# Kernel tuning notes

Hardware: AMD Instinct MI355X
Metric: run time of the kernel (lower is better)

## Reference

```python
import jax, jax.numpy as jnp
import numpy as np

N = 50000
E = 800000
NFEAT = 128
NHID = 32
HEADS = 8
NCLASS = 40


def _gat_conv(x, src, dst, W, att_src, att_dst, bias, concat):
    # x: [N, Fin]; W: [Fin, H*C]; att_*: [H, C]; bias: [H*C] or [C]
    n = x.shape[0]
    H, C = att_src.shape
    h = (x @ W).reshape(n, H, C)                      # [N,H,C]
    a_src = (h * att_src[None]).sum(-1)               # [N,H]
    a_dst = (h * att_dst[None]).sum(-1)               # [N,H]
    e = jax.nn.leaky_relu(a_src[src] + a_dst[dst], 0.2)  # [E,H]
    # edge softmax over incoming edges of each dst node
    m = jax.ops.segment_max(e, dst, num_segments=n)   # [N,H]
    e = jnp.exp(e - m[dst])
    s = jax.ops.segment_sum(e, dst, num_segments=n)   # [N,H]
    alpha = e / (s[dst] + 1e-16)                      # [E,H]
    msg = h[src] * alpha[:, :, None]                  # [E,H,C]
    out = jax.ops.segment_sum(msg, dst, num_segments=n)  # [N,H,C]
    if concat:
        out = out.reshape(n, H * C)
    else:
        out = out.mean(axis=1)
    return out + bias


def setup_inputs() -> dict:
    key = jax.random.key(0)
    ks = jax.random.split(key, 10)
    x = jax.random.normal(ks[0], (N, NFEAT), dtype=jnp.float32)
    edge_index = jax.random.randint(ks[1], (2, E), 0, N, dtype=jnp.int64)
    sc = 1.0 / np.sqrt(NFEAT)
    W1 = jax.random.uniform(ks[2], (NFEAT, HEADS * NHID), jnp.float32, -sc, sc)
    a1_src = jax.random.uniform(ks[3], (HEADS, NHID), jnp.float32, -sc, sc)
    a1_dst = jax.random.uniform(ks[4], (HEADS, NHID), jnp.float32, -sc, sc)
    b1 = jnp.zeros((HEADS * NHID,), jnp.float32)
    sc2 = 1.0 / np.sqrt(HEADS * NHID)
    W2 = jax.random.uniform(ks[5], (HEADS * NHID, NCLASS), jnp.float32, -sc2, sc2)
    a2_src = jax.random.uniform(ks[6], (1, NCLASS), jnp.float32, -sc2, sc2)
    a2_dst = jax.random.uniform(ks[7], (1, NCLASS), jnp.float32, -sc2, sc2)
    b2 = jnp.zeros((NCLASS,), jnp.float32)
    return {"x": x, "edge_index": edge_index, "W1": W1, "a1_src": a1_src,
            "a1_dst": a1_dst, "b1": b1, "W2": W2, "a2_src": a2_src,
            "a2_dst": a2_dst, "b2": b2}


def reference(x, edge_index, W1, a1_src, a1_dst, b1, W2, a2_src, a2_dst, b2):
    n = x.shape[0]
    loop = jnp.arange(n, dtype=edge_index.dtype)
    src = jnp.concatenate([edge_index[0], loop])  # add self-loops (PyG default)
    dst = jnp.concatenate([edge_index[1], loop])
    # dropout layers are identity in eval mode
    h = jax.nn.elu(_gat_conv(x, src, dst, W1, a1_src, a1_dst, b1, concat=True))
    out = _gat_conv(h, src, dst, W2, a2_src, a2_dst, b2, concat=False)
    return jax.nn.log_softmax(out, axis=1)
```

## Files before the change

### kernel.cpp

```cpp
#include <hip/hip_runtime.h>
#include <math.h>

#define NFEAT  128
#define HC     256
#define HEADS  8
#define NHID   32
#define NCLASS 40

#define INV_LN2 1.44269504088896340736f

typedef unsigned int  uint;
typedef unsigned short ushort;
typedef unsigned char uchar;

typedef __attribute__((ext_vector_type(8))) short bf16x8;
typedef __attribute__((ext_vector_type(4))) float f32x4;
typedef __attribute__((ext_vector_type(2))) float f32x2;

union U8 { uint4 u; bf16x8 v; };

__device__ __forceinline__ uint f2bf1(float f) {
    uint b = __float_as_uint(f);
    b += 0x7FFFu + ((b >> 16) & 1u);
    return b >> 16;
}
__device__ __forceinline__ uint packbf(float lo, float hi) {
    return f2bf1(lo) | (f2bf1(hi) << 16);
}

__device__ __forceinline__ uchar f2fp8(float v) {
    return (uchar)(__builtin_amdgcn_cvt_pk_fp8_f32(v, v, 0, false) & 0xFF);
}
__device__ __forceinline__ float fp8tof(uint byte) {
    auto v2 = __builtin_amdgcn_cvt_pk_f32_fp8((int)byte, false);
    return v2[0];
}

__device__ __forceinline__ float bperm(int addr, float v) {
    return __int_as_float(__builtin_amdgcn_ds_bpermute(addr, __float_as_int(v)));
}
__device__ __forceinline__ int bperm_i(int addr, int v) {
    return __builtin_amdgcn_ds_bpermute(addr, v);
}

#define HU 8
#define PREPB 23
__global__ __launch_bounds__(256)
void k_hist_prep(const int* __restrict__ dst, int E, int* deg,
                 int* __restrict__ rank,
                 const float* __restrict__ W1,
                 const float* __restrict__ attS, const float* __restrict__ attD,
                 const float* __restrict__ W2,
                 const float* __restrict__ a2sw, const float* __restrict__ a2dw,
                 ushort* __restrict__ Wb1, ushort* __restrict__ Wb2) {
    int blk = blockIdx.x;
    int t = threadIdx.x;
    if (blk >= PREPB) {
        int tid = (blk - PREPB) * 256 + t;
        int stride = (gridDim.x - PREPB) * 256;
#pragma unroll
        for (int j = 0; j < HU; ++j) {
            int i = tid + j * stride;
            if (i < E) rank[i] = atomicAdd(&deg[dst[i]], 1);
        }
        return;
    }
    float f[8];
    if (blk < 17) {
        int g = blk * 256 + t;
        int lane = g & 63;
        int step = (g >> 6) & 3;
        int tile = g >> 8;
        int k0 = step * 32 + (lane >> 4) * 8;
        if (tile < 16) {
            int ncol = tile * 16 + (lane & 15);
#pragma unroll
            for (int j = 0; j < 8; ++j) f[j] = W1[(size_t)(k0 + j) * HC + ncol];
        } else {
            int cc = lane & 15;
            int h = cc & 7;
            const float* av = (cc < 8) ? attS : attD;
#pragma unroll
            for (int j = 0; j < 8; ++j) {
                const float* wr = W1 + (size_t)(k0 + j) * HC + h * 32;
                float s = 0.f;
#pragma unroll
                for (int c = 0; c < 32; ++c) s += wr[c] * av[h * 32 + c];
                f[j] = s * INV_LN2;
            }
        }
        uint4 o;
        o.x = packbf(f[0], f[1]);
        o.y = packbf(f[2], f[3]);
        o.z = packbf(f[4], f[5]);
        o.w = packbf(f[6], f[7]);
        *(uint4*)(Wb1 + (size_t)g * 8) = o;
    } else {
        int g = (blk - 17) * 256 + t;
        if (g >= 3 * 8 * 64) return;
        int lane = g & 63;
        int ks = (g >> 6) & 7;
        int nt = g >> 9;
        int cc = lane & 15;
        int ncol = nt * 16 + cc;
        int k0 = ks * 32 + (lane >> 4) * 8;
        if (ncol < NCLASS) {
#pragma unroll
            for (int j = 0; j < 8; ++j) f[j] = W2[(size_t)(k0 + j) * NCLASS + ncol];
        } else if (ncol <= 41) {
            const float* av = (ncol == 40) ? a2sw : a2dw;
#pragma unroll
            for (int j = 0; j < 8; ++j) {
                const float* wr = W2 + (size_t)(k0 + j) * NCLASS;
                float s = 0.f;
#pragma unroll
                for (int c = 0; c < NCLASS; ++c) s += wr[c] * av[c];
                f[j] = s * INV_LN2;
            }
        } else {
#pragma unroll
            for (int j = 0; j < 8; ++j) f[j] = 0.f;
        }
        uint4 o;
        o.x = packbf(f[0], f[1]);
        o.y = packbf(f[2], f[3]);
        o.z = packbf(f[4], f[5]);
        o.w = packbf(f[6], f[7]);
        *(uint4*)(Wb2 + (size_t)g * 8) = o;
    }
}

#define SU 4
__global__ __launch_bounds__(256)
void k_scatter_gemm1(const int* __restrict__ srcE, const int* __restrict__ dstE,
                     const int* __restrict__ rank, int E,
                     int* __restrict__ srcs, int scb,
                     const float* __restrict__ x, const ushort* __restrict__ Wb,
                     int n, uchar* __restrict__ h1f8, float* __restrict__ a1x) {
    __shared__ uint Xs[64 * 68];
    int t = threadIdx.x;
    if (blockIdx.x < scb) {
        int tid = blockIdx.x * 256 + t;
        int stride = scb * 256;
        int P = (E + 3) >> 2;
#pragma unroll
        for (int g = 0; g < SU; ++g) {
            int pk = tid + g * stride;
            if (pk >= P) continue;
            int i0 = pk * 4;
            if (i0 + 4 <= E) {
                int4 d4 = *(const int4*)(dstE + i0);
                int4 r4 = *(const int4*)(rank + i0);
                int4 s4 = *(const int4*)(srcE + i0);
                if (r4.x < 64) srcs[((size_t)d4.x << 6) + r4.x] = s4.x;
                if (r4.y < 64) srcs[((size_t)d4.y << 6) + r4.y] = s4.y;
                if (r4.z < 64) srcs[((size_t)d4.z << 6) + r4.z] = s4.z;
                if (r4.w < 64) srcs[((size_t)d4.w << 6) + r4.w] = s4.w;
            } else {
                for (int i = i0; i < E; ++i) {
                    int r = rank[i];
                    if (r < 64) srcs[((size_t)dstE[i] << 6) + r] = srcE[i];
                }
            }
        }
        return;
    }
    int lane = t & 63;
    int w = t >> 6;
    int n0 = (blockIdx.x - scb) * 64;

#pragma unroll
    for (int j = 0; j < 8; ++j) {
        int f4 = t + j * 256;
        int node = f4 >> 5;
        int k4 = (f4 & 31) * 4;
        int gn = n0 + node;
        float4 v = make_float4(0.f, 0.f, 0.f, 0.f);
        if (gn < n) v = *(const float4*)(x + (size_t)gn * NFEAT + k4);
        uint2 pk;
        pk.x = packbf(v.x, v.y);
        pk.y = packbf(v.z, v.w);
        *(uint2*)(Xs + node * 68 + (k4 >> 1)) = pk;
    }
    __syncthreads();

    int m = lane & 15;
    int q4 = (lane >> 4) * 4;
    bf16x8 Af[4];
#pragma unroll
    for (int ks = 0; ks < 4; ++ks) {
        U8 a;
        a.u = *(const uint4*)(Xs + (w * 16 + m) * 68 + ks * 16 + q4);
        Af[ks] = a.v;
    }
    __syncthreads();

    f32x4 acc[17];
#pragma unroll
    for (int i = 0; i < 17; ++i) acc[i] = (f32x4){0.f, 0.f, 0.f, 0.f};

    const bf16x8* Bf = (const bf16x8*)Wb;
#pragma unroll
    for (int ks = 0; ks < 4; ++ks) {
#pragma unroll
        for (int nt = 0; nt < 17; ++nt) {
            bf16x8 bv = Bf[(size_t)(nt * 4 + ks) * 64 + lane];
            acc[nt] = __builtin_amdgcn_mfma_f32_16x16x32_bf16(Af[ks], bv, acc[nt], 0, 0, 0);
        }
    }

    int cc = lane & 15;
    int r0 = (lane >> 4) * 4;

#pragma unroll
    for (int r = 0; r < 4; ++r) {
        int gn = n0 + w * 16 + r0 + r;
        if (gn < n) a1x[(size_t)gn * 16 + cc] = acc[16][r];
    }

    uchar* CsB = (uchar*)Xs;
#pragma unroll
    for (int nt = 0; nt < 16; ++nt) {
#pragma unroll
        for (int r = 0; r < 4; ++r)
            CsB[(w * 16 + r0 + r) * 272 + nt * 16 + cc] = f2fp8(acc[nt][r]);
    }
    __syncthreads();

    int node_local = t >> 2;
    int q = t & 3;
    int gn = n0 + node_local;
    if (gn < n) {
        const uchar* crow = CsB + node_local * 272 + q * 64;
        uchar* hp = h1f8 + (size_t)gn * HC + q * 64;
#pragma unroll
        for (int i = 0; i < 4; ++i)
            *(uint4*)(hp + i * 16) = *(const uint4*)(crow + i * 16);
    }
}

__global__ __launch_bounds__(256)
void k_agg1(const uint* __restrict__ h1u, const float* __restrict__ a1x,
            const float* __restrict__ b1, const int* __restrict__ deg,
            const int* __restrict__ srcs,
            int n, ushort* __restrict__ hgb) {
    int wid = blockIdx.x * 4 + (threadIdx.x >> 6);
    if (wid >= n) return;
    wid = __builtin_amdgcn_readfirstlane(wid);
    int lane = threadIdx.x & 63;
    int vj = lane >> 3;
    int hh = lane & 7;
    int hacc = lane >> 3;
    float adn = a1x[(size_t)wid * 16 + 8 + hh];
    const char* a1xb = (const char*)a1x;
    int ax8  = (lane ^ 8)  << 2;
    int ax16 = (lane ^ 16) << 2;
    int ax32 = (lane ^ 32) << 2;
    int bpc  = hacc << 2;
    int bpp[8];
#pragma unroll
    for (int j = 0; j < 8; ++j) bpp[j] = ((j << 3) + hacc) << 2;

    int degw = __builtin_amdgcn_readfirstlane(deg[wid]);
    degw = (degw < 63) ? degw : 63;
    int cnt = degw + 1;
    int sv_full = srcs[((size_t)wid << 6) + lane];
    int sv_pad = (lane < degw) ? sv_full : wid;

    float s = 0.f;
    f32x2 acc01 = (f32x2){0.f, 0.f};
    f32x2 acc23 = (f32x2){0.f, 0.f};

    struct Chunk { float av; uint hv[8]; };
    Chunk A, B;

#define LOADC1(C, base) do {                                                   \
    int idxl_ = (base) + vj;                                                   \
    int svv_ = bperm_i(idxl_ << 2, sv_pad);                                    \
    (C).av = *(const float*)(a1xb + ((size_t)(uint)svv_ << 6) + ((uint)hh << 2)); \
    _Pragma("unroll")                                                          \
    for (int j_ = 0; j_ < 8; ++j_) {                                           \
        if ((base) + j_ >= cnt) break;                     \
        int sn_ = __builtin_amdgcn_readlane(sv_pad, (base) + j_);              \
        (C).hv[j_] = h1u[(size_t)(uint)sn_ * 64 + lane];                       \
    }                                                                          \
} while (0)

#define CONSC1(C, base) do {                                                   \
    int idxl_ = (base) + vj;                                                   \
    float a_ = (C).av + adn;                                                   \
    float e_ = fmaxf(a_, 0.2f * a_);                                           \
    float p_ = (idxl_ < cnt) ? __builtin_exp2f(e_) : 0.f;                      \
    s += p_;                                                                   \
    _Pragma("unroll")                                                          \
    for (int j_ = 0; j_ < 8; ++j_) {                                           \
        if ((base) + j_ >= cnt) break;                     \
        float pj_ = bperm(bpp[j_], p_);                                        \
        f32x2 pj2_ = (f32x2){pj_, pj_};                                        \
        auto lo_ = __builtin_amdgcn_cvt_pk_f32_fp8((int)(C).hv[j_], false);    \
        auto hi_ = __builtin_amdgcn_cvt_pk_f32_fp8((int)(C).hv[j_], true);     \
        f32x2 lov_ = (f32x2){lo_[0], lo_[1]};                                  \
        f32x2 hiv_ = (f32x2){hi_[0], hi_[1]};                                  \
        acc01 += pj2_ * lov_;                                                  \
        acc23 += pj2_ * hiv_;                                                  \
    }                                                                          \
} while (0)

    int i = 0;
    LOADC1(A, 0);
    while (i + 8 < cnt) {
        LOADC1(B, i + 8);
        CONSC1(A, i);
        i += 8;
        if (i + 8 < cnt) {
            LOADC1(A, i + 8);
            CONSC1(B, i);
            i += 8;
        } else {
            CONSC1(B, i);
            goto tail1;
        }
    }
    CONSC1(A, i);
tail1:;
#undef LOADC1
#undef CONSC1

    float ps = s + bperm(ax8, s);
    ps += bperm(ax16, ps);
    ps += bperm(ax32, ps);
    float inv = 1.f / (ps + 1e-16f);
    float inv_a = bperm(bpc, inv);
    float4 bv = *(const float4*)(b1 + lane * 4);
    float4 o;
    o.x = acc01[0] * inv_a + bv.x;
    o.y = acc01[1] * inv_a + bv.y;
    o.z = acc23[0] * inv_a + bv.z;
    o.w = acc23[1] * inv_a + bv.w;
    o.x = (o.x > 0.f) ? o.x : (__expf(o.x) - 1.f);
    o.y = (o.y > 0.f) ? o.y : (__expf(o.y) - 1.f);
    o.z = (o.z > 0.f) ? o.z : (__expf(o.z) - 1.f);
    o.w = (o.w > 0.f) ? o.w : (__expf(o.w) - 1.f);
    uint2 ov;
    ov.x = packbf(o.x, o.y);
    ov.y = packbf(o.z, o.w);
    *(uint2*)(hgb + (size_t)wid * HC + lane * 4) = ov;
}

__global__ __launch_bounds__(256)
void k_gemm2(const ushort* __restrict__ hgb, const ushort* __restrict__ Wb2,
             int n, uchar* __restrict__ h2f8) {
    __shared__ uint Xs[64 * 132];
    int t = threadIdx.x;
    int lane = t & 63;
    int w = t >> 6;
    int n0 = blockIdx.x * 64;

#pragma unroll
    for (int j = 0; j < 8; ++j) {
        int g = t + j * 256;
        int node = g >> 5;
        int u4 = g & 31;
        int gn = n0 + node;
        uint4 v = make_uint4(0u, 0u, 0u, 0u);
        if (gn < n) v = *(const uint4*)(hgb + (size_t)gn * HC + u4 * 8);
        *(uint4*)(Xs + node * 132 + u4 * 4) = v;
    }
    __syncthreads();

    int m = lane & 15;
    int q4 = (lane >> 4) * 4;
    bf16x8 Af[8];
#pragma unroll
    for (int ks = 0; ks < 8; ++ks) {
        U8 a;
        a.u = *(const uint4*)(Xs + (w * 16 + m) * 132 + ks * 16 + q4);
        Af[ks] = a.v;
    }
    __syncthreads();

    f32x4 acc[3];
#pragma unroll
    for (int i = 0; i < 3; ++i) acc[i] = (f32x4){0.f, 0.f, 0.f, 0.f};

    const bf16x8* Bf = (const bf16x8*)Wb2;
#pragma unroll
    for (int ks = 0; ks < 8; ++ks) {
#pragma unroll
        for (int nt = 0; nt < 3; ++nt) {
            bf16x8 bv = Bf[(size_t)(nt * 8 + ks) * 64 + lane];
            acc[nt] = __builtin_amdgcn_mfma_f32_16x16x32_bf16(Af[ks], bv, acc[nt], 0, 0, 0);
        }
    }

    int cc = lane & 15;
    int r0 = (lane >> 4) * 4;

    uchar* CsB = (uchar*)Xs;
#pragma unroll
    for (int nt = 0; nt < 2; ++nt) {
#pragma unroll
        for (int r = 0; r < 4; ++r)
            CsB[(w * 16 + r0 + r) * 64 + nt * 16 + cc] = f2fp8(acc[nt][r]);
    }
#pragma unroll
    for (int r = 0; r < 4; ++r) {
        int row = (w * 16 + r0 + r) * 64;
        if (cc < 8)       CsB[row + 32 + cc] = f2fp8(acc[2][r]);
        else if (cc == 8) *(float*)(CsB + row + 40) = acc[2][r];
        else if (cc == 9) *(float*)(CsB + row + 44) = acc[2][r];
        else if (cc == 10) *(uint*)(CsB + row + 48) = 0u;
        else if (cc == 11) *(uint*)(CsB + row + 52) = 0u;
        else if (cc == 12) *(uint*)(CsB + row + 56) = 0u;
        else if (cc == 13) *(uint*)(CsB + row + 60) = 0u;
    }
    __syncthreads();

    int node_local = t >> 2;
    int q = t & 3;
    int gn = n0 + node_local;
    if (gn < n)
        *(uint4*)(h2f8 + (size_t)gn * 64 + q * 16) =
            *(const uint4*)(CsB + node_local * 64 + q * 16);
}

__global__ __launch_bounds__(256)
void k_agg2(const uchar* __restrict__ h2f8, const float* __restrict__ b2,
            const int* __restrict__ deg, const int* __restrict__ srcs,
            int n, float* __restrict__ out) {
    int wid = blockIdx.x * 4 + (threadIdx.x >> 6);
    if (wid >= n) return;
    wid = __builtin_amdgcn_readfirstlane(wid);
    int lane = threadIdx.x & 63;
    int vj = lane & 7;
    bool live = lane < NCLASS;
    int col = live ? lane : 0;
    const char* h2b = (const char*)h2f8;
    float adn = *(const float*)(h2b + (size_t)wid * 64 + 44);
    int ax1 = (lane ^ 1) << 2;
    int ax2 = (lane ^ 2) << 2;
    int ax4 = (lane ^ 4) << 2;
    int bpj[8];
#pragma unroll
    for (int j = 0; j < 8; ++j) bpj[j] = j << 2;

    int degw = __builtin_amdgcn_readfirstlane(deg[wid]);
    degw = (degw < 63) ? degw : 63;
    int cnt = degw + 1;
    int sv_full = srcs[((size_t)wid << 6) + lane];
    int sv_pad = (lane < degw) ? sv_full : wid;

    float s = 0.f, acc = 0.f;

    struct Chunk2 { float av; uint hb[8]; };
    Chunk2 A, B;

#define LOADC2(C, base) do {                                                   \
    int idxl_ = (base) + vj;                                                   \
    int svv_ = bperm_i(idxl_ << 2, sv_pad);                                    \
    (C).av = *(const float*)(h2b + ((size_t)(uint)svv_ << 6) + 40u);           \
    _Pragma("unroll")                                                          \
    for (int j_ = 0; j_ < 8; ++j_) {                                           \
        if ((base) + j_ >= cnt) break;                     \
        int sn_ = __builtin_amdgcn_readlane(sv_pad, (base) + j_);              \
        (C).hb[j_] = h2f8[(size_t)(uint)sn_ * 64 + col];                       \
    }                                                                          \
} while (0)

#define CONSC2(C, base) do {                                                   \
    int idxl_ = (base) + vj;                                                   \
    float a_ = (C).av + adn;                                                   \
    float e_ = fmaxf(a_, 0.2f * a_);                                           \
    float p_ = (idxl_ < cnt) ? __builtin_exp2f(e_) : 0.f;                      \
    s += p_;                                                                   \
    _Pragma("unroll")                                                          \
    for (int j_ = 0; j_ < 8; ++j_) {                                           \
        if ((base) + j_ >= cnt) break;                     \
        float pj_ = bperm(bpj[j_], p_);                                        \
        acc += pj_ * fp8tof((C).hb[j_]);                                       \
    }                                                                          \
} while (0)

    int i = 0;
    LOADC2(A, 0);
    while (i + 8 < cnt) {
        LOADC2(B, i + 8);
        CONSC2(A, i);
        i += 8;
        if (i + 8 < cnt) {
            LOADC2(A, i + 8);
            CONSC2(B, i);
            i += 8;
        } else {
            CONSC2(B, i);
            goto tail2;
        }
    }
    CONSC2(A, i);
tail2:;
#undef LOADC2
#undef CONSC2

    float ps = s + bperm(ax1, s);
    ps += bperm(ax2, ps);
    ps += bperm(ax4, ps);

    float val0 = acc / (ps + 1e-16f) + (live ? b2[lane] : 0.f);
    float vmax = live ? val0 : -INFINITY;
#pragma unroll
    for (int msk = 1; msk < 64; msk <<= 1) vmax = fmaxf(vmax, __shfl_xor(vmax, msk, 64));
    float ex = live ? __expf(val0 - vmax) : 0.f;
#pragma unroll
    for (int msk = 1; msk < 64; msk <<= 1) ex += __shfl_xor(ex, msk, 64);
    float res = val0 - vmax - __logf(ex);
    if (live) out[(size_t)wid * NCLASS + lane] = res;
}

extern "C" void kernel_launch(void* const* d_in, const int* in_sizes, int n_in,
                              void* d_out, int out_size, void* d_ws, size_t ws_size,
                              hipStream_t stream) {
    const float* x    = (const float*)d_in[0];
    const int*   ei   = (const int*)  d_in[1];
    const float* W1   = (const float*)d_in[2];
    const float* attS = (const float*)d_in[3];
    const float* attD = (const float*)d_in[4];
    const float* b1   = (const float*)d_in[5];
    const float* W2   = (const float*)d_in[6];
    const float* a2sw = (const float*)d_in[7];
    const float* a2dw = (const float*)d_in[8];
    const float* b2   = (const float*)d_in[9];

    int n = in_sizes[0] / NFEAT;
    int E = in_sizes[1] / 2;
    const int* srcE = ei;
    const int* dstE = ei + E;
    int mblocks = (n + 63) / 64;

    char* p = (char*)d_ws;
    auto alloc = [&](size_t bytes) {
        char* r = p;
        p += (bytes + 255) & ~(size_t)255;
        return r;
    };
    uchar*  h1f8 = (uchar*)alloc((size_t)n * HC);
    ushort* hgb  = (ushort*)alloc((size_t)n * HC * 2);
    uchar*  h2f8 = (uchar*)alloc((size_t)n * 64);
    ushort* Wb1  = (ushort*)alloc((size_t)17 * 4 * 64 * 8 * 2);
    ushort* Wb2  = (ushort*)alloc((size_t)3 * 8 * 64 * 8 * 2);
    float* a1x = (float*)alloc((size_t)n * 16 * 4);
    int* deg  = (int*)alloc((size_t)n * 4);
    int* rank = (int*)alloc((size_t)E * 4);
    int* srcs = (int*)alloc((size_t)n * 64 * 4);

    int histb = (E + 256 * HU - 1) / (256 * HU);
    int P = (E + 3) / 4;
    int scb = (P + 256 * SU - 1) / (256 * SU);
    hipMemsetAsync(deg, 0, (size_t)n * 4, stream);
    k_hist_prep<<<PREPB + histb, 256, 0, stream>>>(dstE, E, deg, rank,
                                                   W1, attS, attD, W2, a2sw, a2dw,
                                                   Wb1, Wb2);
    k_scatter_gemm1<<<scb + mblocks, 256, 0, stream>>>(
        srcE, dstE, rank, E, srcs, scb, x, Wb1, n, h1f8, a1x);
    k_agg1<<<(n + 3) / 4, 256, 0, stream>>>((const uint*)h1f8, a1x, b1,
                                            deg, srcs, n, hgb);
    k_gemm2<<<mblocks, 256, 0, stream>>>(hgb, Wb2, n, h2f8);
    k_agg2<<<(n + 3) / 4, 256, 0, stream>>>(h2f8, b2, deg, srcs, n, (float*)d_out);
}
```

Before: 226.5 us.

## Fuse histogram and scatter into a partitioned single pass; triple-buffer aggregation loads

Replaces the two-pass edge bucketing (an atomic histogram that writes ranks, then a separate scatter pass) with one pass. Each block group owns one eighth of the destination-node range, so atomics and srcs writes stay local, and the rank array is removed. The scatter is split out of the GEMM1 launch into its own gemm1 kernel. Both aggregation kernels move from double to triple buffering of neighbor chunks with prefetch two ahead, and the per-element count-break checks are dropped because padded lanes carry self indices. The cost is that every group re-reads the whole edge list, eight reads in total, and the extra chunk buffer adds register pressure.

```diff
diff --git a/kernel.cpp b/kernel.cpp
--- a/kernel.cpp
+++ b/kernel.cpp
@@ -43,11 +43,12 @@
     return __builtin_amdgcn_ds_bpermute(addr, v);
 }
 
-#define HU 8
+
 #define PREPB 23
+#define SCG 125
 __global__ __launch_bounds__(256)
-void k_hist_prep(const int* __restrict__ dst, int E, int* deg,
-                 int* __restrict__ rank,
+void k_hist_prep(const int* __restrict__ srcE, const int* __restrict__ dstE,
+                 int E, int n, int* deg, int* __restrict__ srcs,
                  const float* __restrict__ W1,
                  const float* __restrict__ attS, const float* __restrict__ attD,
                  const float* __restrict__ W2,
@@ -56,12 +57,43 @@
     int blk = blockIdx.x;
     int t = threadIdx.x;
     if (blk >= PREPB) {
-        int tid = (blk - PREPB) * 256 + t;
-        int stride = (gridDim.x - PREPB) * 256;
-#pragma unroll
-        for (int j = 0; j < HU; ++j) {
-            int i = tid + j * stride;
-            if (i < E) rank[i] = atomicAdd(&deg[dst[i]], 1);
+        int sb = blk - PREPB;
+        int g = blk & 7;
+        int q = sb >> 3;
+        int rs = (n + 7) >> 3;
+        int lo = g * rs;
+        int span = n - lo; if (span > rs) span = rs;
+        int P = (E + 3) >> 2;
+        for (int p = q * 256 + t; p < P; p += SCG * 256) {
+            int i0 = p * 4;
+            if (i0 + 4 <= E) {
+                int4 d4 = *(const int4*)(dstE + i0);
+                int4 s4 = *(const int4*)(srcE + i0);
+                if ((uint)(d4.x - lo) < (uint)span) {
+                    int sl = atomicAdd(&deg[d4.x], 1);
+                    if (sl < 64) srcs[((size_t)d4.x << 6) + sl] = s4.x;
+                }
+                if ((uint)(d4.y - lo) < (uint)span) {
+                    int sl = atomicAdd(&deg[d4.y], 1);
+                    if (sl < 64) srcs[((size_t)d4.y << 6) + sl] = s4.y;
+                }
+                if ((uint)(d4.z - lo) < (uint)span) {
+                    int sl = atomicAdd(&deg[d4.z], 1);
+                    if (sl < 64) srcs[((size_t)d4.z << 6) + sl] = s4.z;
+                }
+                if ((uint)(d4.w - lo) < (uint)span) {
+                    int sl = atomicAdd(&deg[d4.w], 1);
+                    if (sl < 64) srcs[((size_t)d4.w << 6) + sl] = s4.w;
+                }
+            } else {
+                for (int i = i0; i < E; ++i) {
+                    int d = dstE[i];
+                    if ((uint)(d - lo) < (uint)span) {
+                        int sl = atomicAdd(&deg[d], 1);
+                        if (sl < 64) srcs[((size_t)d << 6) + sl] = srcE[i];
+                    }
+                }
+            }
         }
         return;
     }
@@ -130,44 +162,14 @@
     }
 }
 
-#define SU 4
 __global__ __launch_bounds__(256)
-void k_scatter_gemm1(const int* __restrict__ srcE, const int* __restrict__ dstE,
-                     const int* __restrict__ rank, int E,
-                     int* __restrict__ srcs, int scb,
-                     const float* __restrict__ x, const ushort* __restrict__ Wb,
-                     int n, uchar* __restrict__ h1f8, float* __restrict__ a1x) {
+void k_gemm1(const float* __restrict__ x, const ushort* __restrict__ Wb,
+             int n, uchar* __restrict__ h1f8, float* __restrict__ a1x) {
     __shared__ uint Xs[64 * 68];
     int t = threadIdx.x;
-    if (blockIdx.x < scb) {
-        int tid = blockIdx.x * 256 + t;
-        int stride = scb * 256;
-        int P = (E + 3) >> 2;
-#pragma unroll
-        for (int g = 0; g < SU; ++g) {
-            int pk = tid + g * stride;
-            if (pk >= P) continue;
-            int i0 = pk * 4;
-            if (i0 + 4 <= E) {
-                int4 d4 = *(const int4*)(dstE + i0);
-                int4 r4 = *(const int4*)(rank + i0);
-                int4 s4 = *(const int4*)(srcE + i0);
-                if (r4.x < 64) srcs[((size_t)d4.x << 6) + r4.x] = s4.x;
-                if (r4.y < 64) srcs[((size_t)d4.y << 6) + r4.y] = s4.y;
-                if (r4.z < 64) srcs[((size_t)d4.z << 6) + r4.z] = s4.z;
-                if (r4.w < 64) srcs[((size_t)d4.w << 6) + r4.w] = s4.w;
-            } else {
-                for (int i = i0; i < E; ++i) {
-                    int r = rank[i];
-                    if (r < 64) srcs[((size_t)dstE[i] << 6) + r] = srcE[i];
-                }
-            }
-        }
-        return;
-    }
     int lane = t & 63;
     int w = t >> 6;
-    int n0 = (blockIdx.x - scb) * 64;
+    int n0 = blockIdx.x * 64;
 
 #pragma unroll
     for (int j = 0; j < 8; ++j) {
@@ -272,7 +274,7 @@
     f32x2 acc23 = (f32x2){0.f, 0.f};
 
     struct Chunk { float av; uint hv[8]; };
-    Chunk A, B;
+    Chunk X, Y, Z;
 
 #define LOADC1(C, base) do {                                                   \
     int idxl_ = (base) + vj;                                                   \
@@ -280,7 +282,6 @@
     (C).av = *(const float*)(a1xb + ((size_t)(uint)svv_ << 6) + ((uint)hh << 2)); \
     _Pragma("unroll")                                                          \
     for (int j_ = 0; j_ < 8; ++j_) {                                           \
-        if ((base) + j_ >= cnt) break;                     \
         int sn_ = __builtin_amdgcn_readlane(sv_pad, (base) + j_);              \
         (C).hv[j_] = h1u[(size_t)(uint)sn_ * 64 + lane];                       \
     }                                                                          \
@@ -294,7 +295,6 @@
     s += p_;                                                                   \
     _Pragma("unroll")                                                          \
     for (int j_ = 0; j_ < 8; ++j_) {                                           \
-        if ((base) + j_ >= cnt) break;                     \
         float pj_ = bperm(bpp[j_], p_);                                        \
         f32x2 pj2_ = (f32x2){pj_, pj_};                                        \
         auto lo_ = __builtin_amdgcn_cvt_pk_f32_fp8((int)(C).hv[j_], false);    \
@@ -306,23 +306,22 @@
     }                                                                          \
 } while (0)
 
-    int i = 0;
-    LOADC1(A, 0);
-    while (i + 8 < cnt) {
-        LOADC1(B, i + 8);
-        CONSC1(A, i);
-        i += 8;
-        if (i + 8 < cnt) {
-            LOADC1(A, i + 8);
-            CONSC1(B, i);
-            i += 8;
-        } else {
-            CONSC1(B, i);
-            goto tail1;
-        }
-    }
-    CONSC1(A, i);
-tail1:;
+    {
+        int i = 0;
+        LOADC1(X, 0);
+        if (8 < cnt) LOADC1(Y, 8);
+        while (true) {
+            if (i + 16 < cnt) LOADC1(Z, i + 16);
+            CONSC1(X, i);
+            i += 8; if (i >= cnt) break;
+            if (i + 16 < cnt) LOADC1(X, i + 16);
+            CONSC1(Y, i);
+            i += 8; if (i >= cnt) break;
+            if (i + 16 < cnt) LOADC1(Y, i + 16);
+            CONSC1(Z, i);
+            i += 8; if (i >= cnt) break;
+        }
+    }
 #undef LOADC1
 #undef CONSC1
 
@@ -453,7 +452,7 @@
     float s = 0.f, acc = 0.f;
 
     struct Chunk2 { float av; uint hb[8]; };
-    Chunk2 A, B;
+    Chunk2 X, Y, Z;
 
 #define LOADC2(C, base) do {                                                   \
     int idxl_ = (base) + vj;                                                   \
@@ -461,7 +460,6 @@
     (C).av = *(const float*)(h2b + ((size_t)(uint)svv_ << 6) + 40u);           \
     _Pragma("unroll")                                                          \
     for (int j_ = 0; j_ < 8; ++j_) {                                           \
-        if ((base) + j_ >= cnt) break;                     \
         int sn_ = __builtin_amdgcn_readlane(sv_pad, (base) + j_);              \
         (C).hb[j_] = h2f8[(size_t)(uint)sn_ * 64 + col];                       \
     }                                                                          \
@@ -475,29 +473,27 @@
     s += p_;                                                                   \
     _Pragma("unroll")                                                          \
     for (int j_ = 0; j_ < 8; ++j_) {                                           \
-        if ((base) + j_ >= cnt) break;                     \
         float pj_ = bperm(bpj[j_], p_);                                        \
         acc += pj_ * fp8tof((C).hb[j_]);                                       \
     }                                                                          \
 } while (0)
 
-    int i = 0;
-    LOADC2(A, 0);
-    while (i + 8 < cnt) {
-        LOADC2(B, i + 8);
-        CONSC2(A, i);
-        i += 8;
-        if (i + 8 < cnt) {
-            LOADC2(A, i + 8);
-            CONSC2(B, i);
-            i += 8;
-        } else {
-            CONSC2(B, i);
-            goto tail2;
-        }
-    }
-    CONSC2(A, i);
-tail2:;
+    {
+        int i = 0;
+        LOADC2(X, 0);
+        if (8 < cnt) LOADC2(Y, 8);
+        while (true) {
+            if (i + 16 < cnt) LOADC2(Z, i + 16);
+            CONSC2(X, i);
+            i += 8; if (i >= cnt) break;
+            if (i + 16 < cnt) LOADC2(X, i + 16);
+            CONSC2(Y, i);
+            i += 8; if (i >= cnt) break;
+            if (i + 16 < cnt) LOADC2(Y, i + 16);
+            CONSC2(Z, i);
+            i += 8; if (i >= cnt) break;
+        }
+    }
 #undef LOADC2
 #undef CONSC2
 
@@ -549,18 +545,13 @@
     ushort* Wb2  = (ushort*)alloc((size_t)3 * 8 * 64 * 8 * 2);
     float* a1x = (float*)alloc((size_t)n * 16 * 4);
     int* deg  = (int*)alloc((size_t)n * 4);
-    int* rank = (int*)alloc((size_t)E * 4);
     int* srcs = (int*)alloc((size_t)n * 64 * 4);
 
-    int histb = (E + 256 * HU - 1) / (256 * HU);
-    int P = (E + 3) / 4;
-    int scb = (P + 256 * SU - 1) / (256 * SU);
     hipMemsetAsync(deg, 0, (size_t)n * 4, stream);
-    k_hist_prep<<<PREPB + histb, 256, 0, stream>>>(dstE, E, deg, rank,
-                                                   W1, attS, attD, W2, a2sw, a2dw,
-                                                   Wb1, Wb2);
-    k_scatter_gemm1<<<scb + mblocks, 256, 0, stream>>>(
-        srcE, dstE, rank, E, srcs, scb, x, Wb1, n, h1f8, a1x);
+    k_hist_prep<<<PREPB + 8 * SCG, 256, 0, stream>>>(srcE, dstE, E, n, deg, srcs,
+                                                     W1, attS, attD, W2, a2sw, a2dw,
+                                                     Wb1, Wb2);
+    k_gemm1<<<mblocks, 256, 0, stream>>>(x, Wb1, n, h1f8, a1x);
     k_agg1<<<(n + 3) / 4, 256, 0, stream>>>((const uint*)h1f8, a1x, b1,
                                             deg, srcs, n, hgb);
     k_gemm2<<<mblocks, 256, 0, stream>>>(hgb, Wb2, n, h2f8);
```

Result: no change. 230.3 us (+1.7%).

## Fuse layer-1 aggregation with layer-2 GEMM via shared-memory tile

Applied to the files above, without the earlier changes.

Merges the layer-1 aggregation kernel and the layer-2 GEMM into one 1024-thread kernel. Each of 16 waves aggregates 4 nodes into an LDS tile of 64 bf16 rows, then 4 waves run the MFMA GEMM on that tile and write h2f8 directly. This removes the bf16 intermediate buffer round-trip through global memory and one launch. In exchange, 12 of the 16 waves sit idle during the GEMM phase and occupancy may drop with the large blocks. It also removes the early-break guards in the unrolled gather loops, so every chunk now issues all 8 loads using padded self indices, which is extra memory traffic for low-degree nodes.

```diff
diff --git a/kernel.cpp b/kernel.cpp
--- a/kernel.cpp
+++ b/kernel.cpp
@@ -42,6 +42,7 @@
 __device__ __forceinline__ int bperm_i(int addr, int v) {
     return __builtin_amdgcn_ds_bpermute(addr, v);
 }
+
 
 #define HU 8
 #define PREPB 23
@@ -239,19 +240,20 @@
     }
 }
 
-__global__ __launch_bounds__(256)
-void k_agg1(const uint* __restrict__ h1u, const float* __restrict__ a1x,
-            const float* __restrict__ b1, const int* __restrict__ deg,
-            const int* __restrict__ srcs,
-            int n, ushort* __restrict__ hgb) {
-    int wid = blockIdx.x * 4 + (threadIdx.x >> 6);
-    if (wid >= n) return;
-    wid = __builtin_amdgcn_readfirstlane(wid);
-    int lane = threadIdx.x & 63;
+__global__ __launch_bounds__(1024)
+void k_agg1_gemm2(const uint* __restrict__ h1u, const float* __restrict__ a1x,
+                  const float* __restrict__ b1, const int* __restrict__ deg,
+                  const int* __restrict__ srcs, const ushort* __restrict__ Wb2,
+                  int n, uchar* __restrict__ h2f8) {
+    __shared__ uint Xs[64 * 132];
+    int t = threadIdx.x;
+    int lane = t & 63;
+    int w = t >> 6;
+    int n0 = blockIdx.x * 64;
+
     int vj = lane >> 3;
     int hh = lane & 7;
     int hacc = lane >> 3;
-    float adn = a1x[(size_t)wid * 16 + 8 + hh];
     const char* a1xb = (const char*)a1x;
     int ax8  = (lane ^ 8)  << 2;
     int ax16 = (lane ^ 16) << 2;
@@ -260,19 +262,26 @@
     int bpp[8];
 #pragma unroll
     for (int j = 0; j < 8; ++j) bpp[j] = ((j << 3) + hacc) << 2;
-
-    int degw = __builtin_amdgcn_readfirstlane(deg[wid]);
-    degw = (degw < 63) ? degw : 63;
-    int cnt = degw + 1;
-    int sv_full = srcs[((size_t)wid << 6) + lane];
-    int sv_pad = (lane < degw) ? sv_full : wid;
-
-    float s = 0.f;
-    f32x2 acc01 = (f32x2){0.f, 0.f};
-    f32x2 acc23 = (f32x2){0.f, 0.f};
-
-    struct Chunk { float av; uint hv[8]; };
-    Chunk A, B;
+    float4 bv = *(const float4*)(b1 + lane * 4);
+
+    for (int k = 0; k < 4; ++k) {
+        int node_local = w * 4 + k;
+        int wid = n0 + node_local;
+        if (wid < n) {
+            wid = __builtin_amdgcn_readfirstlane(wid);
+            float adn = a1x[(size_t)wid * 16 + 8 + hh];
+            int degw = __builtin_amdgcn_readfirstlane(deg[wid]);
+            degw = (degw < 63) ? degw : 63;
+            int cnt = degw + 1;
+            int sv_full = srcs[((size_t)wid << 6) + lane];
+            int sv_pad = (lane < degw) ? sv_full : wid;
+
+            float s = 0.f;
+            f32x2 acc01 = (f32x2){0.f, 0.f};
+            f32x2 acc23 = (f32x2){0.f, 0.f};
+
+            struct Chunk { float av; uint hv[8]; };
+            Chunk A, B;
 
 #define LOADC1(C, base) do {                                                   \
     int idxl_ = (base) + vj;                                                   \
@@ -280,7 +289,6 @@
     (C).av = *(const float*)(a1xb + ((size_t)(uint)svv_ << 6) + ((uint)hh << 2)); \
     _Pragma("unroll")                                                          \
     for (int j_ = 0; j_ < 8; ++j_) {                                           \
-        if ((base) + j_ >= cnt) break;                     \
         int sn_ = __builtin_amdgcn_readlane(sv_pad, (base) + j_);              \
         (C).hv[j_] = h1u[(size_t)(uint)sn_ * 64 + lane];                       \
     }                                                                          \
@@ -294,7 +302,6 @@
     s += p_;                                                                   \
     _Pragma("unroll")                                                          \
     for (int j_ = 0; j_ < 8; ++j_) {                                           \
-        if ((base) + j_ >= cnt) break;                     \
         float pj_ = bperm(bpp[j_], p_);                                        \
         f32x2 pj2_ = (f32x2){pj_, pj_};                                        \
         auto lo_ = __builtin_amdgcn_cvt_pk_f32_fp8((int)(C).hv[j_], false);    \
@@ -306,122 +313,112 @@
     }                                                                          \
 } while (0)
 
-    int i = 0;
-    LOADC1(A, 0);
-    while (i + 8 < cnt) {
-        LOADC1(B, i + 8);
-        CONSC1(A, i);
-        i += 8;
-        if (i + 8 < cnt) {
-            LOADC1(A, i + 8);
-            CONSC1(B, i);
-            i += 8;
-        } else {
-            CONSC1(B, i);
-            goto tail1;
-        }
-    }
-    CONSC1(A, i);
-tail1:;
+            {
+                int i = 0;
+                LOADC1(A, 0);
+                while (i + 8 < cnt) {
+                    LOADC1(B, i + 8);
+                    CONSC1(A, i);
+                    i += 8;
+                    if (i + 8 < cnt) {
+                        LOADC1(A, i + 8);
+                        CONSC1(B, i);
+                        i += 8;
+                    } else {
+                        CONSC1(B, i);
+                        goto done1;
+                    }
+                }
+                CONSC1(A, i);
+done1:;
+            }
 #undef LOADC1
 #undef CONSC1
 
-    float ps = s + bperm(ax8, s);
-    ps += bperm(ax16, ps);
-    ps += bperm(ax32, ps);
-    float inv = 1.f / (ps + 1e-16f);
-    float inv_a = bperm(bpc, inv);
-    float4 bv = *(const float4*)(b1 + lane * 4);
-    float4 o;
-    o.x = acc01[0] * inv_a + bv.x;
-    o.y = acc01[1] * inv_a + bv.y;
-    o.z = acc23[0] * inv_a + bv.z;
-    o.w = acc23[1] * inv_a + bv.w;
-    o.x = (o.x > 0.f) ? o.x : (__expf(o.x) - 1.f);
-    o.y = (o.y > 0.f) ? o.y : (__expf(o.y) - 1.f);
-    o.z = (o.z > 0.f) ? o.z : (__expf(o.z) - 1.f);
-    o.w = (o.w > 0.f) ? o.w : (__expf(o.w) - 1.f);
-    uint2 ov;
-    ov.x = packbf(o.x, o.y);
-    ov.y = packbf(o.z, o.w);
-    *(uint2*)(hgb + (size_t)wid * HC + lane * 4) = ov;
-}
-
-__global__ __launch_bounds__(256)
-void k_gemm2(const ushort* __restrict__ hgb, const ushort* __restrict__ Wb2,
-             int n, uchar* __restrict__ h2f8) {
-    __shared__ uint Xs[64 * 132];
-    int t = threadIdx.x;
-    int lane = t & 63;
-    int w = t >> 6;
-    int n0 = blockIdx.x * 64;
-
-#pragma unroll
-    for (int j = 0; j < 8; ++j) {
-        int g = t + j * 256;
-        int node = g >> 5;
-        int u4 = g & 31;
-        int gn = n0 + node;
-        uint4 v = make_uint4(0u, 0u, 0u, 0u);
-        if (gn < n) v = *(const uint4*)(hgb + (size_t)gn * HC + u4 * 8);
-        *(uint4*)(Xs + node * 132 + u4 * 4) = v;
+            float ps = s + bperm(ax8, s);
+            ps += bperm(ax16, ps);
+            ps += bperm(ax32, ps);
+            float inv = 1.f / (ps + 1e-16f);
+            float inv_a = bperm(bpc, inv);
+            float4 o;
+            o.x = acc01[0] * inv_a + bv.x;
+            o.y = acc01[1] * inv_a + bv.y;
+            o.z = acc23[0] * inv_a + bv.z;
+            o.w = acc23[1] * inv_a + bv.w;
+            o.x = (o.x > 0.f) ? o.x : (__expf(o.x) - 1.f);
+            o.y = (o.y > 0.f) ? o.y : (__expf(o.y) - 1.f);
+            o.z = (o.z > 0.f) ? o.z : (__expf(o.z) - 1.f);
+            o.w = (o.w > 0.f) ? o.w : (__expf(o.w) - 1.f);
+            uint2 ov;
+            ov.x = packbf(o.x, o.y);
+            ov.y = packbf(o.z, o.w);
+            *(uint2*)(Xs + node_local * 132 + lane * 2) = ov;
+        } else {
+            *(uint2*)(Xs + node_local * 132 + lane * 2) = make_uint2(0u, 0u);
+        }
     }
     __syncthreads();
 
     int m = lane & 15;
     int q4 = (lane >> 4) * 4;
     bf16x8 Af[8];
-#pragma unroll
-    for (int ks = 0; ks < 8; ++ks) {
-        U8 a;
-        a.u = *(const uint4*)(Xs + (w * 16 + m) * 132 + ks * 16 + q4);
-        Af[ks] = a.v;
+    if (w < 4) {
+#pragma unroll
+        for (int ks = 0; ks < 8; ++ks) {
+            U8 a;
+            a.u = *(const uint4*)(Xs + (w * 16 + m) * 132 + ks * 16 + q4);
+            Af[ks] = a.v;
+        }
     }
     __syncthreads();
 
-    f32x4 acc[3];
-#pragma unroll
-    for (int i = 0; i < 3; ++i) acc[i] = (f32x4){0.f, 0.f, 0.f, 0.f};
-
-    const bf16x8* Bf = (const bf16x8*)Wb2;
-#pragma unroll
-    for (int ks = 0; ks < 8; ++ks) {
-#pragma unroll
-        for (int nt = 0; nt < 3; ++nt) {
-            bf16x8 bv = Bf[(size_t)(nt * 8 + ks) * 64 + lane];
-            acc[nt] = __builtin_amdgcn_mfma_f32_16x16x32_bf16(Af[ks], bv, acc[nt], 0, 0, 0);
-        }
-    }
-
-    int cc = lane & 15;
-    int r0 = (lane >> 4) * 4;
-
-    uchar* CsB = (uchar*)Xs;
-#pragma unroll
-    for (int nt = 0; nt < 2; ++nt) {
-#pragma unroll
-        for (int r = 0; r < 4; ++r)
-            CsB[(w * 16 + r0 + r) * 64 + nt * 16 + cc] = f2fp8(acc[nt][r]);
-    }
-#pragma unroll
-    for (int r = 0; r < 4; ++r) {
-        int row = (w * 16 + r0 + r) * 64;
-        if (cc < 8)       CsB[row + 32 + cc] = f2fp8(acc[2][r]);
-        else if (cc == 8) *(float*)(CsB + row + 40) = acc[2][r];
-        else if (cc == 9) *(float*)(CsB + row + 44) = acc[2][r];
-        else if (cc == 10) *(uint*)(CsB + row + 48) = 0u;
-        else if (cc == 11) *(uint*)(CsB + row + 52) = 0u;
-        else if (cc == 12) *(uint*)(CsB + row + 56) = 0u;
-        else if (cc == 13) *(uint*)(CsB + row + 60) = 0u;
+    if (w < 4) {
+        f32x4 acc[3];
+#pragma unroll
+        for (int i = 0; i < 3; ++i) acc[i] = (f32x4){0.f, 0.f, 0.f, 0.f};
+
+        const bf16x8* Bf = (const bf16x8*)Wb2;
+#pragma unroll
+        for (int ks = 0; ks < 8; ++ks) {
+#pragma unroll
+            for (int nt = 0; nt < 3; ++nt) {
+                bf16x8 bvv = Bf[(size_t)(nt * 8 + ks) * 64 + lane];
+                acc[nt] = __builtin_amdgcn_mfma_f32_16x16x32_bf16(Af[ks], bvv, acc[nt], 0, 0, 0);
+            }
+        }
+
+        int cc = lane & 15;
+        int r0 = (lane >> 4) * 4;
+        uchar* CsB = (uchar*)Xs;
+#pragma unroll
+        for (int nt = 0; nt < 2; ++nt) {
+#pragma unroll
+            for (int r = 0; r < 4; ++r)
+                CsB[(w * 16 + r0 + r) * 64 + nt * 16 + cc] = f2fp8(acc[nt][r]);
+        }
+#pragma unroll
+        for (int r = 0; r < 4; ++r) {
+            int row = (w * 16 + r0 + r) * 64;
+            if (cc < 8)       CsB[row + 32 + cc] = f2fp8(acc[2][r]);
+            else if (cc == 8) *(float*)(CsB + row + 40) = acc[2][r];
+            else if (cc == 9) *(float*)(CsB + row + 44) = acc[2][r];
+            else if (cc == 10) *(uint*)(CsB + row + 48) = 0u;
+            else if (cc == 11) *(uint*)(CsB + row + 52) = 0u;
+            else if (cc == 12) *(uint*)(CsB + row + 56) = 0u;
+            else if (cc == 13) *(uint*)(CsB + row + 60) = 0u;
+        }
     }
     __syncthreads();
 
-    int node_local = t >> 2;
-    int q = t & 3;
-    int gn = n0 + node_local;
-    if (gn < n)
-        *(uint4*)(h2f8 + (size_t)gn * 64 + q * 16) =
-            *(const uint4*)(CsB + node_local * 64 + q * 16);
+    if (t < 256) {
+        const uchar* CsB = (const uchar*)Xs;
+        int node_local = t >> 2;
+        int q = t & 3;
+        int gn = n0 + node_local;
+        if (gn < n)
+            *(uint4*)(h2f8 + (size_t)gn * 64 + q * 16) =
+                *(const uint4*)(CsB + node_local * 64 + q * 16);
+    }
 }
 
 __global__ __launch_bounds__(256)
@@ -461,7 +458,6 @@
     (C).av = *(const float*)(h2b + ((size_t)(uint)svv_ << 6) + 40u);           \
     _Pragma("unroll")                                                          \
     for (int j_ = 0; j_ < 8; ++j_) {                                           \
-        if ((base) + j_ >= cnt) break;                     \
         int sn_ = __builtin_amdgcn_readlane(sv_pad, (base) + j_);              \
         (C).hb[j_] = h2f8[(size_t)(uint)sn_ * 64 + col];                       \
     }                                                                          \
@@ -475,7 +471,6 @@
     s += p_;                                                                   \
     _Pragma("unroll")                                                          \
     for (int j_ = 0; j_ < 8; ++j_) {                                           \
-        if ((base) + j_ >= cnt) break;                     \
         float pj_ = bperm(bpj[j_], p_);                                        \
         acc += pj_ * fp8tof((C).hb[j_]);                                       \
     }                                                                          \
@@ -543,7 +538,6 @@
         return r;
     };
     uchar*  h1f8 = (uchar*)alloc((size_t)n * HC);
-    ushort* hgb  = (ushort*)alloc((size_t)n * HC * 2);
     uchar*  h2f8 = (uchar*)alloc((size_t)n * 64);
     ushort* Wb1  = (ushort*)alloc((size_t)17 * 4 * 64 * 8 * 2);
     ushort* Wb2  = (ushort*)alloc((size_t)3 * 8 * 64 * 8 * 2);
@@ -561,8 +555,7 @@
                                                    Wb1, Wb2);
     k_scatter_gemm1<<<scb + mblocks, 256, 0, stream>>>(
         srcE, dstE, rank, E, srcs, scb, x, Wb1, n, h1f8, a1x);
-    k_agg1<<<(n + 3) / 4, 256, 0, stream>>>((const uint*)h1f8, a1x, b1,
-                                            deg, srcs, n, hgb);
-    k_gemm2<<<mblocks, 256, 0, stream>>>(hgb, Wb2, n, h2f8);
+    k_agg1_gemm2<<<mblocks, 1024, 0, stream>>>((const uint*)h1f8, a1x, b1,
+                                               deg, srcs, Wb2, n, h2f8);
     k_agg2<<<(n + 3) / 4, 256, 0, stream>>>(h2f8, b2, deg, srcs, n, (float*)d_out);
 }
```

After: 239.3 us. 5.6% more time.
